# Performance work log

Hardware: AMD Instinct MI355X
Metric: run time of the kernel (lower is better)

Reference implementation:

```python
import jax, jax.numpy as jnp
import numpy as np

N = 10000          # nodes
E = 160000         # directed edges (before self loops)
H = 6              # GATConv heads (hardcoded in init_conv)
D = 128            # in_channels = hidden = out_channels
L = 4              # len(hidden_dims) + 1 conv layers
NEG_SLOPE = 0.2    # GATConv default leaky_relu slope


def setup_inputs() -> dict:
    key = jax.random.key(0)
    ks = jax.random.split(key, 2 + 4 * L)
    inp = {}
    inp["x"] = jax.random.normal(ks[0], (N, D), dtype=jnp.float32)
    inp["edge_index"] = jax.random.randint(ks[1], (2, E), 0, N, dtype=jnp.int64)
    for i in range(L):
        kW, ka, kb, kbias = jax.random.split(ks[2 + i], 4)
        scale = 1.0 / np.sqrt(D)
        inp[f"W{i}"] = jax.random.normal(kW, (D, H * D), dtype=jnp.float32) * scale
        inp[f"att_src{i}"] = jax.random.normal(ka, (1, H, D), dtype=jnp.float32) * scale
        inp[f"att_dst{i}"] = jax.random.normal(kb, (1, H, D), dtype=jnp.float32) * scale
        inp[f"b{i}"] = jnp.zeros((D,), dtype=jnp.float32)
    return inp


def _gat_layer(x, src, dst, W, att_src, att_dst, bias):
    # x: [N, Din]; src/dst: [E'] (with self loops); W: [Din, H*C]
    n = x.shape[0]
    xw = (x @ W).reshape(n, H, -1)                      # [N, H, C]
    a_src = jnp.sum(xw * att_src, axis=-1)              # [N, H]
    a_dst = jnp.sum(xw * att_dst, axis=-1)              # [N, H]
    e = jax.nn.leaky_relu(a_src[src] + a_dst[dst], NEG_SLOPE)  # [E', H]
    # segment softmax over edges grouped by destination node
    m = jax.lax.stop_gradient(jax.ops.segment_max(e, dst, num_segments=n))
    e = jnp.exp(e - m[dst])
    denom = jax.ops.segment_sum(e, dst, num_segments=n)  # [N, H]
    alpha = e / (denom[dst] + 1e-16)                     # [E', H]
    out = jax.ops.segment_sum(alpha[:, :, None] * xw[src], dst, num_segments=n)  # [N, H, C]
    return jnp.mean(out, axis=1) + bias                  # concat=False -> head mean


def reference(x, edge_index,
              W0, att_src0, att_dst0, b0,
              W1, att_src1, att_dst1, b1,
              W2, att_src2, att_dst2, b2,
              W3, att_src3, att_dst3, b3):
    n = x.shape[0]
    loops = jnp.arange(n, dtype=edge_index.dtype)
    src = jnp.concatenate([edge_index[0], loops])  # add_self_loops=True
    dst = jnp.concatenate([edge_index[1], loops])
    params = [(W0, att_src0, att_dst0, b0), (W1, att_src1, att_dst1, b1),
              (W2, att_src2, att_dst2, b2), (W3, att_src3, att_dst3, b3)]
    for (W, a_s, a_d, b) in params:
        x = _gat_layer(x, src, dst, W, a_s, a_d, b)
        x = jax.nn.relu(x)  # norm=Identity, dropout eval/no-op; relu applied every layer (jk_mode set)
    return x
```

## Files before the change

### kernel.cpp

```cpp
#include <hip/hip_runtime.h>
#include <hip/hip_fp16.h>
#include <math.h>

#define H 6
#define D 128
#define K_ALL (H * D)
#define TSTEPS 24
#define PADK 776
#define NPB 8
#define BSTRIDE 128

typedef _Float16 f16x8 __attribute__((ext_vector_type(8)));
typedef float f32x4 __attribute__((ext_vector_type(4)));

struct FoldArgs {
    const float* W[4];
    const float* as[4];
    const float* ad[4];
};


__global__ __launch_bounds__(256) void zero_wa_kernel(int4* __restrict__ degz, int n4,
                                                      int zBlocks, FoldArgs fa,
                                                      float* __restrict__ wa_all) {
    int b = blockIdx.x;
    int tid = threadIdx.x;
    if (b < zBlocks) {
        int i = b * 256 + tid;
        if (i < n4) degz[i] = make_int4(0, 0, 0, 0);
        return;
    }
    int t = (b - zBlocks) * 256 + tid;
    if (t >= 4 * 1536) return;
    int l = t / 1536;
    int r = t % 1536;
    int k = r / 12, j = r % 12;
    int h = (j < 6) ? j : (j - 6);
    const float* att = (j < 6) ? fa.as[l] : fa.ad[l];
    const float* wrow = fa.W[l] + (size_t)k * K_ALL + h * D;
    const float* arow = att + h * D;
    float s = 0.f;
    #pragma unroll 8
    for (int c = 0; c < D; c++) s += wrow[c] * arow[c];
    wa_all[(size_t)l * 1536 + k * 12 + j] = s;
}


__global__ __launch_bounds__(256) void prep2_kernel(const int* __restrict__ src,
                                                    const int* __restrict__ dst,
                                                    int* __restrict__ deg,
                                                    int* __restrict__ col, int E,
                                                    int scatBlocks, FoldArgs fa,
                                                    const float* __restrict__ wa_all,
                                                    _Float16* __restrict__ waf,
                                                    _Float16* __restrict__ bf,
                                                    const float* __restrict__ x_in,
                                                    float* __restrict__ a0, int N) {
    __shared__ _Float16 xs[16][136];
    int b = blockIdx.x;
    int tid = threadIdx.x;
    if (b < scatBlocks) {
        int e = b * 256 + tid;
        if (e < E) {
            int n = dst[e];
            int p = atomicAdd(&deg[n], 1);
            if (p < BSTRIDE) col[(size_t)n * BSTRIDE + p] = src[e];
        }
        return;
    }
    int bb = b - scatBlocks;
    if (bb < 192) {
        int idx = bb * 256 + tid;
        int l63 = idx & 63;
        int ct = (idx >> 6) & 7;
        int t = (idx >> 9) % TSTEPS;
        int layer = idx / (TSTEPS * 8 * 64);
        const float* W = fa.W[layer];
        int c = ct * 16 + (l63 & 15);
        f16x8 v;
        #pragma unroll
        for (int j = 0; j < 8; j++) {
            int k = t * 32 + ((l63 >> 4) << 3) + j;
            v[j] = (_Float16)W[(size_t)(k & 127) * K_ALL + ((k >> 7) << 7) + c];
        }
        *(f16x8*)(bf + ((size_t)idx << 3)) = v;
        return;
    }
    bb -= 192;
    if (bb < 4) {
        int L = bb;
        int lane = tid & 63;
        int t = tid >> 6;
        int j = lane & 15;
        const float* wl = wa_all + (size_t)L * 1536;
        f16x8 vv;
        #pragma unroll
        for (int jj = 0; jj < 8; jj++) {
            int k = t * 32 + ((lane >> 4) << 3) + jj;
            float sv = (j < 12) ? wl[k * 12 + j] : 0.f;
            vv[jj] = (_Float16)sv;
        }
        *(f16x8*)(waf + (size_t)L * 2048 + (size_t)t * 512 + (size_t)lane * 8) = vv;
        return;
    }
    bb -= 4;
    int base_node = bb << 4;
    {
        int row = tid >> 4;
        int coff = (tid & 15) * 8;
        int node = base_node + row;
        f16x8 v = {};
        if (node < N) {
            const float* sp = x_in + (size_t)node * D + coff;
            float4 u0 = *(const float4*)sp;
            float4 u1 = *(const float4*)(sp + 4);
            v[0] = (_Float16)u0.x; v[1] = (_Float16)u0.y;
            v[2] = (_Float16)u0.z; v[3] = (_Float16)u0.w;
            v[4] = (_Float16)u1.x; v[5] = (_Float16)u1.y;
            v[6] = (_Float16)u1.z; v[7] = (_Float16)u1.w;
        }
        *(f16x8*)&xs[row][coff] = v;
    }
    __syncthreads();
    if (tid < 64) {
        int lane = tid;
        int cl = lane & 15;
        int r0 = (lane >> 4) << 2;
        const float* wl0 = wa_all;
        f32x4 ac = {0.f, 0.f, 0.f, 0.f};
        #pragma unroll
        for (int t = 0; t < 4; t++) {
            f16x8 av = *(const f16x8*)&xs[cl][t * 32 + ((lane >> 4) << 3)];
            f16x8 bv;
            #pragma unroll
            for (int jj = 0; jj < 8; jj++) {
                int k = t * 32 + ((lane >> 4) << 3) + jj;
                float sv = (cl < 12) ? wl0[k * 12 + cl] : 0.f;
                bv[jj] = (_Float16)sv;
            }
            ac = __builtin_amdgcn_mfma_f32_16x16x32_f16(av, bv, ac, 0, 0, 0);
        }
        if (cl < 12) {
            #pragma unroll
            for (int reg = 0; reg < 4; reg++) {
                int node = base_node + r0 + reg;
                if (node < N) a0[(size_t)node * 12 + cl] = ac[reg];
            }
        }
    }
}

__device__ __forceinline__ float rlf(float v, int j) {
    return __int_as_float(__builtin_amdgcn_readlane(__float_as_int(v), j));
}

__device__ __forceinline__ void aggregate_node(const float* __restrict__ x,
                                               const float* __restrict__ a,
                                               const int* __restrict__ deg_,
                                               const int* __restrict__ col,
                                               int n, int lane, int Nn,
                                               _Float16* __restrict__ xsrow) {
    const int deg = deg_[n];
    const int start = n << 7;
    int colv = col[start + lane];
    const int nent = deg + 1;

    if (nent <= 64) {
        int sc = ((unsigned)colv < (unsigned)Nn) ? colv : n;
        int s = (lane < deg) ? sc : n;

        const float* xb = x + (lane << 1);
        float2 cur0, cur1, nxt0, nxt1;
        {
            int t0 = __builtin_amdgcn_readlane(s, 0);
            cur0 = *(const float2*)(xb + (size_t)t0 * D);
        }
        cur1 = make_float2(0.f, 0.f);
        nxt0 = make_float2(0.f, 0.f);
        nxt1 = make_float2(0.f, 0.f);
        if (nent > 1) {
            int t1 = __builtin_amdgcn_readlane(s, 1);
            cur1 = *(const float2*)(xb + (size_t)t1 * D);
        }
        if (nent > 2) {
            int t2 = __builtin_amdgcn_readlane(s, 2);
            nxt0 = *(const float2*)(xb + (size_t)t2 * D);
        }
        if (nent > 3) {
            int t3 = __builtin_amdgcn_readlane(s, 3);
            nxt1 = *(const float2*)(xb + (size_t)t3 * D);
        }

        float adst[H];
        #pragma unroll
        for (int h = 0; h < H; h++) adst[h] = a[(size_t)n * 12 + 6 + h];
        const float* as_ = a + (size_t)s * 12;
        float4 v0 = *(const float4*)as_;
        float2 v1 = *(const float2*)(as_ + 4);
        float e0 = v0.x + adst[0], e1 = v0.y + adst[1], e2 = v0.z + adst[2];
        float e3 = v0.w + adst[3], e4 = v1.x + adst[4], e5 = v1.y + adst[5];
        e0 = e0 > 0.f ? e0 : 0.2f * e0;  e1 = e1 > 0.f ? e1 : 0.2f * e1;
        e2 = e2 > 0.f ? e2 : 0.2f * e2;  e3 = e3 > 0.f ? e3 : 0.2f * e3;
        e4 = e4 > 0.f ? e4 : 0.2f * e4;  e5 = e5 > 0.f ? e5 : 0.2f * e5;
        float w0 = __expf(e0), w1 = __expf(e1), w2 = __expf(e2);
        float w3 = __expf(e3), w4 = __expf(e4), w5 = __expf(e5);

        float d0 = 0, d1 = 0, d2 = 0, d3 = 0, d4 = 0, d5 = 0;
        float a00 = 0, a01 = 0, a02 = 0, a03 = 0, a04 = 0, a05 = 0;
        float a10 = 0, a11 = 0, a12 = 0, a13 = 0, a14 = 0, a15 = 0;

        for (int j = 0; j < nent; j += 2) {
            float2 fut0 = make_float2(0.f, 0.f), fut1 = make_float2(0.f, 0.f);
            if (j + 4 < nent) {
                int t = __builtin_amdgcn_readlane(s, j + 4);
                fut0 = *(const float2*)(xb + (size_t)t * D);
            }
            if (j + 5 < nent) {
                int t = __builtin_amdgcn_readlane(s, j + 5);
                fut1 = *(const float2*)(xb + (size_t)t * D);
            }
            {
                float b0 = rlf(w0, j), b1 = rlf(w1, j), b2 = rlf(w2, j);
                float b3 = rlf(w3, j), b4 = rlf(w4, j), b5 = rlf(w5, j);
                d0 += b0; d1 += b1; d2 += b2; d3 += b3; d4 += b4; d5 += b5;
                a00 += b0 * cur0.x; a10 += b0 * cur0.y;
                a01 += b1 * cur0.x; a11 += b1 * cur0.y;
                a02 += b2 * cur0.x; a12 += b2 * cur0.y;
                a03 += b3 * cur0.x; a13 += b3 * cur0.y;
                a04 += b4 * cur0.x; a14 += b4 * cur0.y;
                a05 += b5 * cur0.x; a15 += b5 * cur0.y;
            }
            if (j + 1 < nent) {
                float b0 = rlf(w0, j + 1), b1 = rlf(w1, j + 1), b2 = rlf(w2, j + 1);
                float b3 = rlf(w3, j + 1), b4 = rlf(w4, j + 1), b5 = rlf(w5, j + 1);
                d0 += b0; d1 += b1; d2 += b2; d3 += b3; d4 += b4; d5 += b5;
                a00 += b0 * cur1.x; a10 += b0 * cur1.y;
                a01 += b1 * cur1.x; a11 += b1 * cur1.y;
                a02 += b2 * cur1.x; a12 += b2 * cur1.y;
                a03 += b3 * cur1.x; a13 += b3 * cur1.y;
                a04 += b4 * cur1.x; a14 += b4 * cur1.y;
                a05 += b5 * cur1.x; a15 += b5 * cur1.y;
            }
            cur0 = nxt0; cur1 = nxt1;
            nxt0 = fut0; nxt1 = fut1;
        }
        float i0 = 1.f / d0, i1 = 1.f / d1, i2 = 1.f / d2;
        float i3 = 1.f / d3, i4 = 1.f / d4, i5 = 1.f / d5;
        int c = lane << 1;
        xsrow[0 * D + c] = (_Float16)(a00 * i0);  xsrow[0 * D + c + 1] = (_Float16)(a10 * i0);
        xsrow[1 * D + c] = (_Float16)(a01 * i1);  xsrow[1 * D + c + 1] = (_Float16)(a11 * i1);
        xsrow[2 * D + c] = (_Float16)(a02 * i2);  xsrow[2 * D + c + 1] = (_Float16)(a12 * i2);
        xsrow[3 * D + c] = (_Float16)(a03 * i3);  xsrow[3 * D + c + 1] = (_Float16)(a13 * i3);
        xsrow[4 * D + c] = (_Float16)(a04 * i4);  xsrow[4 * D + c + 1] = (_Float16)(a14 * i4);
        xsrow[5 * D + c] = (_Float16)(a05 * i5);  xsrow[5 * D + c + 1] = (_Float16)(a15 * i5);
    } else {
        float adst[H];
        #pragma unroll
        for (int h = 0; h < H; h++) adst[h] = a[(size_t)n * 12 + 6 + h];
        int dl = deg < BSTRIDE ? deg : BSTRIDE;
        float d[H] = {0, 0, 0, 0, 0, 0};
        float acc0[H] = {0, 0, 0, 0, 0, 0};
        float acc1[H] = {0, 0, 0, 0, 0, 0};
        int c0 = lane, c1 = 64 + lane;
        for (int j = 0; j <= dl; j++) {
            int s = (j < dl) ? col[start + j] : n;
            float w[H];
            #pragma unroll
            for (int h = 0; h < H; h++) {
                float e = a[(size_t)s * 12 + h] + adst[h];
                e = (e > 0.f) ? e : 0.2f * e;
                w[h] = __expf(e);
                d[h] += w[h];
            }
            float xv0 = x[(size_t)s * D + c0];
            float xv1 = x[(size_t)s * D + c1];
            #pragma unroll
            for (int h = 0; h < H; h++) {
                acc0[h] += w[h] * xv0;
                acc1[h] += w[h] * xv1;
            }
        }
        #pragma unroll
        for (int h = 0; h < H; h++) {
            float inv = 1.0f / d[h];
            xsrow[h * D + c0] = (_Float16)(acc0[h] * inv);
            xsrow[h * D + c1] = (_Float16)(acc1[h] * inv);
        }
    }
}

__global__ __launch_bounds__(512) void layer_kernel(const float* __restrict__ x,
                                                    const float* __restrict__ a_in,
                                                    const int* __restrict__ deg_,
                                                    const int* __restrict__ col,
                                                    const _Float16* __restrict__ bf,
                                                    const float* __restrict__ bias,
                                                    float* __restrict__ xout,
                                                    const _Float16* __restrict__ awf,
                                                    float* __restrict__ a_out, int M) {
    __shared__ _Float16 xs16[16][PADK];
    __shared__ _Float16 xso[16][136];
    const int wave = (int)(threadIdx.x >> 6);
    const int lane = (int)(threadIdx.x & 63);
    const int m0 = (int)(blockIdx.x << 3);

    {
        int n = m0 + wave;
        if (n < M)
            aggregate_node(x, a_in, deg_, col, n, lane, M, &xs16[wave][0]);
    }
    __syncthreads();

    f32x4 acc = {0.f, 0.f, 0.f, 0.f};
    const _Float16* ars = &xs16[lane & 15][(lane >> 4) << 3];
    const _Float16* bp = bf + (size_t)wave * 512 + (size_t)lane * 8;
    for (int t = 0; t < TSTEPS; t++) {
        f16x8 av = *(const f16x8*)(ars + t * 32);
        f16x8 bv = *(const f16x8*)(bp + (size_t)t * 4096);
        acc = __builtin_amdgcn_mfma_f32_16x16x32_f16(av, bv, acc, 0, 0, 0);
    }

    const float inv6 = 1.0f / 6.0f;
    const int cl = lane & 15;
    const int ccol = wave * 16 + cl;
    const int r0 = (lane >> 4) << 2;
    const float bs = bias[ccol];
    #pragma unroll
    for (int reg = 0; reg < 4; reg++) {
        int ml = r0 + reg;
        int m = m0 + ml;
        float v = acc[reg] * inv6 + bs;
        v = v > 0.f ? v : 0.f;
        if (ml < NPB && m < M) xout[(size_t)m * D + ccol] = v;
        xso[ml][ccol] = (_Float16)v;
    }

    if (awf) {
        __syncthreads();
        if (wave == 0) {
            f32x4 ac = {0.f, 0.f, 0.f, 0.f};
            #pragma unroll
            for (int t = 0; t < 4; t++) {
                f16x8 av = *(const f16x8*)&xso[cl][t * 32 + ((lane >> 4) << 3)];
                f16x8 bv = *(const f16x8*)(awf + (size_t)t * 512 + (size_t)lane * 8);
                ac = __builtin_amdgcn_mfma_f32_16x16x32_f16(av, bv, ac, 0, 0, 0);
            }
            if (cl < 12) {
                #pragma unroll
                for (int reg = 0; reg < 4; reg++) {
                    int ml = r0 + reg;
                    int m = m0 + ml;
                    if (ml < NPB && m < M) a_out[(size_t)m * 12 + cl] = ac[reg];
                }
            }
        }
    }
}


extern "C" void kernel_launch(void* const* d_in, const int* in_sizes, int n_in,
                              void* d_out, int out_size, void* d_ws, size_t ws_size,
                              hipStream_t stream) {
    const float* x_in = (const float*)d_in[0];
    const int* ei = (const int*)d_in[1];
    int N = in_sizes[0] / D;
    int E = in_sizes[1] / 2;
    const int* srcp = ei;
    const int* dstp = ei + E;

    size_t bf_halves_per_layer = (size_t)TSTEPS * 8 * 512;

    float* ws = (float*)d_ws;
    float* bufA = ws;
    float* bufB = bufA + (size_t)N * D;
    float* abuf0 = bufB + (size_t)N * D;
    float* abuf1 = abuf0 + (size_t)N * 12;
    float* wa_all = abuf1 + (size_t)N * 12;
    _Float16* waf = (_Float16*)(wa_all + 4 * 1536);
    _Float16* w16f = waf + 4 * 2048;
    int* deg = (int*)(w16f + 4 * bf_halves_per_layer);
    int* col = deg + N;

    FoldArgs fa;
    for (int l = 0; l < 4; l++) {
        fa.W[l]  = (const float*)d_in[2 + 4 * l];
        fa.as[l] = (const float*)d_in[3 + 4 * l];
        fa.ad[l] = (const float*)d_in[4 + 4 * l];
    }

    int n4 = (N + 3) / 4;
    int zBlocks = (n4 + 255) / 256;
    zero_wa_kernel<<<zBlocks + 24, 256, 0, stream>>>((int4*)deg, n4, zBlocks, fa, wa_all);

    int scatBlocks = (E + 255) / 256;
    int a0Blocks = (N + 15) / 16;
    prep2_kernel<<<scatBlocks + 192 + 4 + a0Blocks, 256, 0, stream>>>(
        srcp, dstp, deg, col, E, scatBlocks, fa, wa_all, waf, w16f, x_in, abuf0, N);

    const float* xcur = x_in;
    float* acur = abuf0;
    float* anext = abuf1;
    for (int l = 0; l < 4; l++) {
        const float* b = (const float*)d_in[5 + 4 * l];
        float* xout = (l == 3) ? (float*)d_out : ((l & 1) ? bufB : bufA);
        const _Float16* awf = (l < 3) ? (waf + (size_t)(l + 1) * 2048) : (const _Float16*)nullptr;

        layer_kernel<<<(N + NPB - 1) / NPB, 512, 0, stream>>>(xcur, acur, deg, col,
                                                              w16f + (size_t)l * bf_halves_per_layer,
                                                              b, xout, awf, anext, N);
        xcur = xout;
        float* tmp = acur; acur = anext; anext = tmp;
    }
}
```

Baseline: 131.4 us.

## Split per-node edge aggregation across two waves and combine partials in LDS

Each node's neighbor aggregation is now split across two waves, each handling half of the incoming edges. Partial numerators and denominators are reduced through shared memory before the MFMA projection. The block grows from 512 to 1024 threads, and the fast path now covers nodes with up to 128 entries instead of 64. This shortens the serial gather chain per node, at the cost of extra LDS traffic, another barrier, and idle waves during the GEMM phase.

Measured after the change: 146.9 us. 11.8% more time.

```diff
diff --git a/kernel.cpp b/kernel.cpp
--- a/kernel.cpp
+++ b/kernel.cpp
@@ -154,20 +154,31 @@
     return __int_as_float(__builtin_amdgcn_readlane(__float_as_int(v), j));
 }
 
-__device__ __forceinline__ void aggregate_node(const float* __restrict__ x,
+struct AggPart {
+    float a00, a01, a02, a03, a04, a05;
+    float a10, a11, a12, a13, a14, a15;
+    float d0, d1, d2, d3, d4, d5;
+};
+
+__device__ __forceinline__ void aggregate_half(const float* __restrict__ x,
                                                const float* __restrict__ a,
                                                const int* __restrict__ deg_,
                                                const int* __restrict__ col,
-                                               int n, int lane, int Nn,
-                                               _Float16* __restrict__ xsrow) {
+                                               int n, int lane, int half, int Nn,
+                                               AggPart& P) {
     const int deg = deg_[n];
     const int start = n << 7;
-    int colv = col[start + lane];
     const int nent = deg + 1;
 
-    if (nent <= 64) {
+    if (nent <= 128) {
+        const int nA = (nent + 1) >> 1;
+        const int base = half ? nA : 0;
+        const int cnt = half ? (nent - nA) : nA;
+        if (cnt <= 0) return;
+        const int idxL = base + lane;
+        int colv = col[start + idxL];
         int sc = ((unsigned)colv < (unsigned)Nn) ? colv : n;
-        int s = (lane < deg) ? sc : n;
+        int s = (idxL < deg) ? sc : n;
 
         const float* xb = x + (lane << 1);
         float2 cur0, cur1, nxt0, nxt1;
@@ -178,15 +189,15 @@
         cur1 = make_float2(0.f, 0.f);
         nxt0 = make_float2(0.f, 0.f);
         nxt1 = make_float2(0.f, 0.f);
-        if (nent > 1) {
+        if (cnt > 1) {
             int t1 = __builtin_amdgcn_readlane(s, 1);
             cur1 = *(const float2*)(xb + (size_t)t1 * D);
         }
-        if (nent > 2) {
+        if (cnt > 2) {
             int t2 = __builtin_amdgcn_readlane(s, 2);
             nxt0 = *(const float2*)(xb + (size_t)t2 * D);
         }
-        if (nent > 3) {
+        if (cnt > 3) {
             int t3 = __builtin_amdgcn_readlane(s, 3);
             nxt1 = *(const float2*)(xb + (size_t)t3 * D);
         }
@@ -205,63 +216,48 @@
         float w0 = __expf(e0), w1 = __expf(e1), w2 = __expf(e2);
         float w3 = __expf(e3), w4 = __expf(e4), w5 = __expf(e5);
 
-        float d0 = 0, d1 = 0, d2 = 0, d3 = 0, d4 = 0, d5 = 0;
-        float a00 = 0, a01 = 0, a02 = 0, a03 = 0, a04 = 0, a05 = 0;
-        float a10 = 0, a11 = 0, a12 = 0, a13 = 0, a14 = 0, a15 = 0;
-
-        for (int j = 0; j < nent; j += 2) {
+        for (int j = 0; j < cnt; j += 2) {
             float2 fut0 = make_float2(0.f, 0.f), fut1 = make_float2(0.f, 0.f);
-            if (j + 4 < nent) {
+            if (j + 4 < cnt) {
                 int t = __builtin_amdgcn_readlane(s, j + 4);
                 fut0 = *(const float2*)(xb + (size_t)t * D);
             }
-            if (j + 5 < nent) {
+            if (j + 5 < cnt) {
                 int t = __builtin_amdgcn_readlane(s, j + 5);
                 fut1 = *(const float2*)(xb + (size_t)t * D);
             }
             {
                 float b0 = rlf(w0, j), b1 = rlf(w1, j), b2 = rlf(w2, j);
                 float b3 = rlf(w3, j), b4 = rlf(w4, j), b5 = rlf(w5, j);
-                d0 += b0; d1 += b1; d2 += b2; d3 += b3; d4 += b4; d5 += b5;
-                a00 += b0 * cur0.x; a10 += b0 * cur0.y;
-                a01 += b1 * cur0.x; a11 += b1 * cur0.y;
-                a02 += b2 * cur0.x; a12 += b2 * cur0.y;
-                a03 += b3 * cur0.x; a13 += b3 * cur0.y;
-                a04 += b4 * cur0.x; a14 += b4 * cur0.y;
-                a05 += b5 * cur0.x; a15 += b5 * cur0.y;
-            }
-            if (j + 1 < nent) {
+                P.d0 += b0; P.d1 += b1; P.d2 += b2; P.d3 += b3; P.d4 += b4; P.d5 += b5;
+                P.a00 += b0 * cur0.x; P.a10 += b0 * cur0.y;
+                P.a01 += b1 * cur0.x; P.a11 += b1 * cur0.y;
+                P.a02 += b2 * cur0.x; P.a12 += b2 * cur0.y;
+                P.a03 += b3 * cur0.x; P.a13 += b3 * cur0.y;
+                P.a04 += b4 * cur0.x; P.a14 += b4 * cur0.y;
+                P.a05 += b5 * cur0.x; P.a15 += b5 * cur0.y;
+            }
+            if (j + 1 < cnt) {
                 float b0 = rlf(w0, j + 1), b1 = rlf(w1, j + 1), b2 = rlf(w2, j + 1);
                 float b3 = rlf(w3, j + 1), b4 = rlf(w4, j + 1), b5 = rlf(w5, j + 1);
-                d0 += b0; d1 += b1; d2 += b2; d3 += b3; d4 += b4; d5 += b5;
-                a00 += b0 * cur1.x; a10 += b0 * cur1.y;
-                a01 += b1 * cur1.x; a11 += b1 * cur1.y;
-                a02 += b2 * cur1.x; a12 += b2 * cur1.y;
-                a03 += b3 * cur1.x; a13 += b3 * cur1.y;
-                a04 += b4 * cur1.x; a14 += b4 * cur1.y;
-                a05 += b5 * cur1.x; a15 += b5 * cur1.y;
+                P.d0 += b0; P.d1 += b1; P.d2 += b2; P.d3 += b3; P.d4 += b4; P.d5 += b5;
+                P.a00 += b0 * cur1.x; P.a10 += b0 * cur1.y;
+                P.a01 += b1 * cur1.x; P.a11 += b1 * cur1.y;
+                P.a02 += b2 * cur1.x; P.a12 += b2 * cur1.y;
+                P.a03 += b3 * cur1.x; P.a13 += b3 * cur1.y;
+                P.a04 += b4 * cur1.x; P.a14 += b4 * cur1.y;
+                P.a05 += b5 * cur1.x; P.a15 += b5 * cur1.y;
             }
             cur0 = nxt0; cur1 = nxt1;
             nxt0 = fut0; nxt1 = fut1;
         }
-        float i0 = 1.f / d0, i1 = 1.f / d1, i2 = 1.f / d2;
-        float i3 = 1.f / d3, i4 = 1.f / d4, i5 = 1.f / d5;
-        int c = lane << 1;
-        xsrow[0 * D + c] = (_Float16)(a00 * i0);  xsrow[0 * D + c + 1] = (_Float16)(a10 * i0);
-        xsrow[1 * D + c] = (_Float16)(a01 * i1);  xsrow[1 * D + c + 1] = (_Float16)(a11 * i1);
-        xsrow[2 * D + c] = (_Float16)(a02 * i2);  xsrow[2 * D + c + 1] = (_Float16)(a12 * i2);
-        xsrow[3 * D + c] = (_Float16)(a03 * i3);  xsrow[3 * D + c + 1] = (_Float16)(a13 * i3);
-        xsrow[4 * D + c] = (_Float16)(a04 * i4);  xsrow[4 * D + c + 1] = (_Float16)(a14 * i4);
-        xsrow[5 * D + c] = (_Float16)(a05 * i5);  xsrow[5 * D + c + 1] = (_Float16)(a15 * i5);
     } else {
+        if (half) return;
         float adst[H];
         #pragma unroll
         for (int h = 0; h < H; h++) adst[h] = a[(size_t)n * 12 + 6 + h];
         int dl = deg < BSTRIDE ? deg : BSTRIDE;
-        float d[H] = {0, 0, 0, 0, 0, 0};
-        float acc0[H] = {0, 0, 0, 0, 0, 0};
-        float acc1[H] = {0, 0, 0, 0, 0, 0};
-        int c0 = lane, c1 = 64 + lane;
+        const float* xb = x + (lane << 1);
         for (int j = 0; j <= dl; j++) {
             int s = (j < dl) ? col[start + j] : n;
             float w[H];
@@ -270,74 +266,110 @@
                 float e = a[(size_t)s * 12 + h] + adst[h];
                 e = (e > 0.f) ? e : 0.2f * e;
                 w[h] = __expf(e);
-                d[h] += w[h];
-            }
-            float xv0 = x[(size_t)s * D + c0];
-            float xv1 = x[(size_t)s * D + c1];
-            #pragma unroll
-            for (int h = 0; h < H; h++) {
-                acc0[h] += w[h] * xv0;
-                acc1[h] += w[h] * xv1;
-            }
-        }
-        #pragma unroll
-        for (int h = 0; h < H; h++) {
-            float inv = 1.0f / d[h];
-            xsrow[h * D + c0] = (_Float16)(acc0[h] * inv);
-            xsrow[h * D + c1] = (_Float16)(acc1[h] * inv);
-        }
-    }
-}
-
-__global__ __launch_bounds__(512) void layer_kernel(const float* __restrict__ x,
-                                                    const float* __restrict__ a_in,
-                                                    const int* __restrict__ deg_,
-                                                    const int* __restrict__ col,
-                                                    const _Float16* __restrict__ bf,
-                                                    const float* __restrict__ bias,
-                                                    float* __restrict__ xout,
-                                                    const _Float16* __restrict__ awf,
-                                                    float* __restrict__ a_out, int M) {
+            }
+            float2 xv = *(const float2*)(xb + (size_t)s * D);
+            P.d0 += w[0]; P.d1 += w[1]; P.d2 += w[2];
+            P.d3 += w[3]; P.d4 += w[4]; P.d5 += w[5];
+            P.a00 += w[0] * xv.x; P.a10 += w[0] * xv.y;
+            P.a01 += w[1] * xv.x; P.a11 += w[1] * xv.y;
+            P.a02 += w[2] * xv.x; P.a12 += w[2] * xv.y;
+            P.a03 += w[3] * xv.x; P.a13 += w[3] * xv.y;
+            P.a04 += w[4] * xv.x; P.a14 += w[4] * xv.y;
+            P.a05 += w[5] * xv.x; P.a15 += w[5] * xv.y;
+        }
+    }
+}
+
+__global__ __launch_bounds__(1024) void layer_kernel(const float* __restrict__ x,
+                                                     const float* __restrict__ a_in,
+                                                     const int* __restrict__ deg_,
+                                                     const int* __restrict__ col,
+                                                     const _Float16* __restrict__ bf,
+                                                     const float* __restrict__ bias,
+                                                     float* __restrict__ xout,
+                                                     const _Float16* __restrict__ awf,
+                                                     float* __restrict__ a_out, int M) {
     __shared__ _Float16 xs16[16][PADK];
     __shared__ _Float16 xso[16][136];
+    __shared__ float pB[8][64][12];
+    __shared__ float dB[8][8];
     const int wave = (int)(threadIdx.x >> 6);
     const int lane = (int)(threadIdx.x & 63);
+    const int nl = wave & 7;
+    const int half = wave >> 3;
     const int m0 = (int)(blockIdx.x << 3);
-
-    {
-        int n = m0 + wave;
-        if (n < M)
-            aggregate_node(x, a_in, deg_, col, n, lane, M, &xs16[wave][0]);
+    const int n = m0 + nl;
+
+    AggPart P = {};
+    if (n < M) aggregate_half(x, a_in, deg_, col, n, lane, half, M, P);
+
+    if (half == 1 && n < M) {
+        float* pp = &pB[nl][lane][0];
+        pp[0] = P.a00;  pp[1] = P.a01;  pp[2] = P.a02;
+        pp[3] = P.a03;  pp[4] = P.a04;  pp[5] = P.a05;
+        pp[6] = P.a10;  pp[7] = P.a11;  pp[8] = P.a12;
+        pp[9] = P.a13;  pp[10] = P.a14; pp[11] = P.a15;
+        if (lane == 0) {
+            dB[nl][0] = P.d0; dB[nl][1] = P.d1; dB[nl][2] = P.d2;
+            dB[nl][3] = P.d3; dB[nl][4] = P.d4; dB[nl][5] = P.d5;
+        }
     }
     __syncthreads();
 
-    f32x4 acc = {0.f, 0.f, 0.f, 0.f};
-    const _Float16* ars = &xs16[lane & 15][(lane >> 4) << 3];
-    const _Float16* bp = bf + (size_t)wave * 512 + (size_t)lane * 8;
-    for (int t = 0; t < TSTEPS; t++) {
-        f16x8 av = *(const f16x8*)(ars + t * 32);
-        f16x8 bv = *(const f16x8*)(bp + (size_t)t * 4096);
-        acc = __builtin_amdgcn_mfma_f32_16x16x32_f16(av, bv, acc, 0, 0, 0);
-    }
-
-    const float inv6 = 1.0f / 6.0f;
-    const int cl = lane & 15;
-    const int ccol = wave * 16 + cl;
-    const int r0 = (lane >> 4) << 2;
-    const float bs = bias[ccol];
-    #pragma unroll
-    for (int reg = 0; reg < 4; reg++) {
-        int ml = r0 + reg;
-        int m = m0 + ml;
-        float v = acc[reg] * inv6 + bs;
-        v = v > 0.f ? v : 0.f;
-        if (ml < NPB && m < M) xout[(size_t)m * D + ccol] = v;
-        xso[ml][ccol] = (_Float16)v;
+    if (half == 0 && n < M) {
+        const float* pp = &pB[nl][lane][0];
+        float a00 = P.a00 + pp[0], a01 = P.a01 + pp[1], a02 = P.a02 + pp[2];
+        float a03 = P.a03 + pp[3], a04 = P.a04 + pp[4], a05 = P.a05 + pp[5];
+        float a10 = P.a10 + pp[6], a11 = P.a11 + pp[7], a12 = P.a12 + pp[8];
+        float a13 = P.a13 + pp[9], a14 = P.a14 + pp[10], a15 = P.a15 + pp[11];
+        float i0 = 1.f / (P.d0 + dB[nl][0]);
+        float i1 = 1.f / (P.d1 + dB[nl][1]);
+        float i2 = 1.f / (P.d2 + dB[nl][2]);
+        float i3 = 1.f / (P.d3 + dB[nl][3]);
+        float i4 = 1.f / (P.d4 + dB[nl][4]);
+        float i5 = 1.f / (P.d5 + dB[nl][5]);
+        _Float16* xsrow = &xs16[nl][0];
+        int c = lane << 1;
+        xsrow[0 * D + c] = (_Float16)(a00 * i0);  xsrow[0 * D + c + 1] = (_Float16)(a10 * i0);
+        xsrow[1 * D + c] = (_Float16)(a01 * i1);  xsrow[1 * D + c + 1] = (_Float16)(a11 * i1);
+        xsrow[2 * D + c] = (_Float16)(a02 * i2);  xsrow[2 * D + c + 1] = (_Float16)(a12 * i2);
+        xsrow[3 * D + c] = (_Float16)(a03 * i3);  xsrow[3 * D + c + 1] = (_Float16)(a13 * i3);
+        xsrow[4 * D + c] = (_Float16)(a04 * i4);  xsrow[4 * D + c + 1] = (_Float16)(a14 * i4);
+        xsrow[5 * D + c] = (_Float16)(a05 * i5);  xsrow[5 * D + c + 1] = (_Float16)(a15 * i5);
+    }
+    __syncthreads();
+
+    if (half == 0) {
+        f32x4 acc = {0.f, 0.f, 0.f, 0.f};
+        const _Float16* ars = &xs16[lane & 15][(lane >> 4) << 3];
+        const _Float16* bp = bf + (size_t)nl * 512 + (size_t)lane * 8;
+        for (int t = 0; t < TSTEPS; t++) {
+            f16x8 av = *(const f16x8*)(ars + t * 32);
+            f16x8 bv = *(const f16x8*)(bp + (size_t)t * 4096);
+            acc = __builtin_amdgcn_mfma_f32_16x16x32_f16(av, bv, acc, 0, 0, 0);
+        }
+
+        const float inv6 = 1.0f / 6.0f;
+        const int cl = lane & 15;
+        const int ccol = nl * 16 + cl;
+        const int r0 = (lane >> 4) << 2;
+        const float bs = bias[ccol];
+        #pragma unroll
+        for (int reg = 0; reg < 4; reg++) {
+            int ml = r0 + reg;
+            int m = m0 + ml;
+            float v = acc[reg] * inv6 + bs;
+            v = v > 0.f ? v : 0.f;
+            if (ml < NPB && m < M) xout[(size_t)m * D + ccol] = v;
+            xso[ml][ccol] = (_Float16)v;
+        }
     }
 
     if (awf) {
         __syncthreads();
         if (wave == 0) {
+            const int cl = lane & 15;
+            const int r0 = (lane >> 4) << 2;
             f32x4 ac = {0.f, 0.f, 0.f, 0.f};
             #pragma unroll
             for (int t = 0; t < 4; t++) {
@@ -405,9 +437,9 @@
         float* xout = (l == 3) ? (float*)d_out : ((l & 1) ? bufB : bufA);
         const _Float16* awf = (l < 3) ? (waf + (size_t)(l + 1) * 2048) : (const _Float16*)nullptr;
 
-        layer_kernel<<<(N + NPB - 1) / NPB, 512, 0, stream>>>(xcur, acur, deg, col,
-                                                              w16f + (size_t)l * bf_halves_per_layer,
-                                                              b, xout, awf, anext, N);
+        layer_kernel<<<(N + NPB - 1) / NPB, 1024, 0, stream>>>(xcur, acur, deg, col,
+                                                               w16f + (size_t)l * bf_halves_per_layer,
+                                                               b, xout, awf, anext, N);
         xcur = xout;
         float* tmp = acur; acur = anext; anext = tmp;
     }
```
